# Optimization experiments

Measured on AMD Instinct MI355X. Metric: run time of the kernel, lower is better.

Reference implementation:

```python
import jax, jax.numpy as jnp
import numpy as np

B, T, C = 4, 2048, 1024
E, TOP_K, DFF = 8, 2, 4096


def setup_inputs() -> dict:
    key = jax.random.key(0)
    ks = jax.random.split(key, 8)
    scale = 0.02
    return {
        "x": jax.random.normal(ks[0], (B, T, C), dtype=jnp.float32),
        "noise": jax.random.normal(ks[1], (B, T, E), dtype=jnp.float32),
        "w_gate": jax.random.normal(ks[2], (C, E), dtype=jnp.float32) * scale,
        "b_gate": jnp.zeros((E,), dtype=jnp.float32),
        "w_noise": jax.random.normal(ks[3], (C, E), dtype=jnp.float32) * scale,
        "b_noise": jnp.zeros((E,), dtype=jnp.float32),
        "w1": jax.random.normal(ks[4], (E, C, DFF), dtype=jnp.float32) * scale,
        "b1": jnp.zeros((E, DFF), dtype=jnp.float32),
        "w2": jax.random.normal(ks[5], (E, DFF, C), dtype=jnp.float32) * scale,
        "b2": jnp.zeros((E, C), dtype=jnp.float32),
    }


def reference(x, noise, w_gate, b_gate, w_noise, b_noise, w1, b1, w2, b2):
    # Noisy top-k router
    clean_logits = jnp.einsum("btc,ce->bte", x, w_gate) + b_gate
    noise_logits = jnp.einsum("btc,ce->bte", x, w_noise) + b_noise
    logits = clean_logits + noise * jax.nn.softplus(noise_logits)  # (B,T,E)
    top_v, top_i = jax.lax.top_k(logits, TOP_K)  # (B,T,K)
    # softmax over sparse (-inf elsewhere) logits == softmax over top-k values
    # scattered back to expert slots
    w_topk = jax.nn.softmax(top_v, axis=-1)  # (B,T,K)
    weights = jnp.einsum("btk,btke->bte", w_topk, jax.nn.one_hot(top_i, E, dtype=x.dtype))

    # Dense-equivalent dispatch/combine: weights are exactly 0 for
    # non-selected experts, so weighted dense compute matches the
    # gather/scatter combine in the original module.
    out = jnp.zeros_like(x)
    n_experts = w1.shape[0]
    for e in range(n_experts):
        h = jax.nn.relu(jnp.einsum("btc,cf->btf", x, w1[e]) + b1[e])
        y = jnp.einsum("btf,fc->btc", h, w2[e]) + b2[e]
        out = out + weights[..., e:e + 1] * y
    return out
```

## Files before the change

### kernel.cpp

```cpp
#include <hip/hip_runtime.h>
#include <hip/hip_bf16.h>
#include <cmath>

#define DEVFN __device__ __forceinline__

typedef __attribute__((ext_vector_type(8))) short short8;
typedef __attribute__((ext_vector_type(4))) float f32x4;

constexpr int C_DIM   = 1024;
constexpr int E_NUM   = 8;
constexpr int DFF_DIM = 4096;
constexpr int NTOK    = 8192;
constexpr int PAD     = 256;
constexpr int MAXROWS = NTOK * 2 + E_NUM * PAD;

DEVFN unsigned short f2bf(float f) {
    __hip_bfloat16 h = __float2bfloat16(f);
    return __builtin_bit_cast(unsigned short, h);
}
DEVFN float bf2f(unsigned short u) {
    return __bfloat162float(__builtin_bit_cast(__hip_bfloat16, u));
}
DEVFN void gload_lds16(const void* g, void* lds) {
    __builtin_amdgcn_global_load_lds(
        (const __attribute__((address_space(1))) unsigned int*)g,
        (__attribute__((address_space(3))) unsigned int*)lds, 16, 0, 0);
}


__global__ void init_kernel(int* meta, int* rowtok,
                            const float* __restrict__ wg, const float* __restrict__ wn,
                            float* __restrict__ wT) {
    int gid = blockIdx.x * 256 + threadIdx.x;
    if (gid < 64) meta[gid] = 0;
    if (gid < MAXROWS) rowtok[gid] = 0;
    if (gid < 16 * C_DIM) {
        int o = gid >> 10, c = gid & 1023;
        wT[gid] = (o < 8) ? wg[c * 8 + o] : wn[c * 8 + (o - 8)];
    }
}

__global__ __launch_bounds__(256) void router_kernel(
    const float* __restrict__ x, const float* __restrict__ noise,
    const float* __restrict__ wT, const float* __restrict__ bg,
    const float* __restrict__ bn, int* meta, int2* tok_e, float2* tok_w) {
    extern __shared__ float swT[];
    int tid = threadIdx.x;
#pragma unroll
    for (int j = 0; j < 16; j++) {
        int idx = (j * 256 + tid) * 4;
        *(float4*)&swT[idx] = *(const float4*)&wT[idx];
    }
    __syncthreads();

    int tt = tid >> 3, sub = tid & 7;
    int tok = blockIdx.x * 32 + tt;
    const float* xr = x + (size_t)tok * C_DIM;

    double acc[16];
#pragma unroll
    for (int o = 0; o < 16; o++) acc[o] = 0.0;

#pragma unroll 4
    for (int i = 0; i < 32; i++) {
        int c = i * 32 + sub * 4;
        float4 xv = *(const float4*)(xr + c);
#pragma unroll
        for (int o = 0; o < 16; o++) {
            float4 wv = *(const float4*)(&swT[o * C_DIM + c]);
            acc[o] += (double)xv.x * (double)wv.x;
            acc[o] += (double)xv.y * (double)wv.y;
            acc[o] += (double)xv.z * (double)wv.z;
            acc[o] += (double)xv.w * (double)wv.w;
        }
    }
#pragma unroll
    for (int s = 1; s <= 4; s <<= 1) {
#pragma unroll
        for (int o = 0; o < 16; o++) acc[o] += __shfl_xor(acc[o], s, 64);
    }
    if (sub == 0) {
        double logit[8];
#pragma unroll
        for (int e = 0; e < 8; e++) {
            double cl = acc[e] + (double)bg[e];
            double nl = acc[8 + e] + (double)bn[e];
            double sp = (nl > 30.0) ? nl : log1p(exp(nl));
            logit[e] = cl + (double)noise[(size_t)tok * 8 + e] * sp;
        }
        int i1 = -1, i2 = -1;
        double v1 = -1e300, v2 = -1e300;
#pragma unroll
        for (int e = 0; e < 8; e++) {
            double v = logit[e];
            if (v > v1) { v2 = v1; i2 = i1; v1 = v; i1 = e; }
            else if (v > v2) { v2 = v; i2 = e; }
        }
        double d = exp(v2 - v1);
        tok_e[tok] = make_int2(i1, i2);
        tok_w[tok] = make_float2((float)(1.0 / (1.0 + d)), (float)(d / (1.0 + d)));
        atomicAdd(&meta[i1], 1);
        atomicAdd(&meta[i2], 1);
    }
}

__global__ void offsets_kernel(int* meta) {
    if (threadIdx.x == 0 && blockIdx.x == 0) {
        int off = 0;
        for (int e = 0; e < 8; e++) {
            meta[16 + e] = off;
            off += (meta[e] + PAD - 1) / PAD * PAD;
            meta[8 + e] = 0;
        }
        meta[24] = off;
    }
}

__global__ void assign_kernel(int* meta, const int2* tok_e,
                              int2* tok_pos, int* rowtok) {
    int t = blockIdx.x * 256 + threadIdx.x;
    int lane = threadIdx.x & 63;
    int2 e = tok_e[t];
    int sel[2] = {e.x, e.y};
    int pos[2];
#pragma unroll
    for (int s = 0; s < 2; s++) {
        int p = 0;
#pragma unroll
        for (int ex = 0; ex < 8; ex++) {
            unsigned long long m = __ballot(sel[s] == ex);
            if (m) {
                int leader = __ffsll((unsigned long long)m) - 1;
                int base = 0;
                if (lane == leader) base = atomicAdd(&meta[8 + ex], (int)__popcll(m));
                base = __shfl(base, leader, 64);
                if (sel[s] == ex)
                    p = meta[16 + ex] + base + (int)__popcll(m & ((1ull << lane) - 1ull));
            }
        }
        pos[s] = p;
        rowtok[p] = t;
    }
    tok_pos[t] = make_int2(pos[0], pos[1]);
}

DEVFN void transpose_body(const float* __restrict__ ine, unsigned short* __restrict__ oute,
                          int R, int S, int r0, int s0, float (*tile)[68]) {
    int tid = threadIdx.x;
    int rr = tid >> 2, cs = (tid & 3) * 16;
    const float4* src = (const float4*)(ine + (size_t)(r0 + rr) * S + s0 + cs);
#pragma unroll
    for (int q = 0; q < 4; q++) *(float4*)&tile[rr][cs + q * 4] = src[q];
    __syncthreads();
    int ss = tid >> 2, rs = (tid & 3) * 16;
    ushort4 o[4];
#pragma unroll
    for (int q = 0; q < 4; q++) {
        ushort4 v;
        v.x = f2bf(tile[rs + q * 4 + 0][ss]);
        v.y = f2bf(tile[rs + q * 4 + 1][ss]);
        v.z = f2bf(tile[rs + q * 4 + 2][ss]);
        v.w = f2bf(tile[rs + q * 4 + 3][ss]);
        o[q] = v;
    }
    ushort4* dst = (ushort4*)(oute + (size_t)(s0 + ss) * R + r0 + rs);
#pragma unroll
    for (int q = 0; q < 4; q++) dst[q] = o[q];
}

constexpr int NB_T1 = (DFF_DIM / 64) * (C_DIM / 64) * E_NUM;
constexpr int NB_T2 = (C_DIM / 64) * (DFF_DIM / 64) * E_NUM;
__global__ __launch_bounds__(256) void prep_kernel(
    const float* __restrict__ w1, unsigned short* __restrict__ w1b,
    const float* __restrict__ w2, unsigned short* __restrict__ w2b,
    const float* __restrict__ x, const int* __restrict__ rowtok,
    unsigned short* __restrict__ Xg) {
    __shared__ float tile[64][68];
    int b = blockIdx.x;
    if (b < NB_T1) {
        int bx = b & 63, by = (b >> 6) & 15, bz = b >> 10;
        transpose_body(w1 + (size_t)bz * C_DIM * DFF_DIM,
                       w1b + (size_t)bz * C_DIM * DFF_DIM,
                       C_DIM, DFF_DIM, by * 64, bx * 64, tile);
        return;
    }
    b -= NB_T1;
    if (b < NB_T2) {
        int bx = b & 15, by = (b >> 4) & 63, bz = b >> 10;
        transpose_body(w2 + (size_t)bz * C_DIM * DFF_DIM,
                       w2b + (size_t)bz * C_DIM * DFF_DIM,
                       DFF_DIM, C_DIM, by * 64, bx * 64, tile);
        return;
    }
    b -= NB_T2;
    int tok = rowtok[b];
    const float4* src = (const float4*)(x + (size_t)tok * C_DIM);
    ushort4* dst = (ushort4*)(Xg + (size_t)b * C_DIM);
    int i = threadIdx.x;
    float4 v = src[i];
    ushort4 o;
    o.x = f2bf(v.x); o.y = f2bf(v.y); o.z = f2bf(v.z); o.w = f2bf(v.w);
    dst[i] = o;
}

template <int KDIM, int KLEN, int NDIM, int MODE>
__global__ __launch_bounds__(512, 2) void gemm8_kernel(
    const unsigned short* __restrict__ A, const unsigned short* __restrict__ Bt,
    const float* __restrict__ bias, unsigned short* __restrict__ OutH,
    unsigned short* __restrict__ OutC0, unsigned short* __restrict__ OutC1,
    const int* __restrict__ meta) {
    extern __shared__ char ldsraw[];

    int nwg = gridDim.x;
    int orig = blockIdx.x;
    int q = nwg >> 3, r8 = nwg & 7;
    int xcd = orig & 7, idx = orig >> 3;
    int wgid = (xcd < r8 ? xcd * (q + 1) : r8 * (q + 1) + (xcd - r8) * q) + idx;
    constexpr int NCT = NDIM / 256;
    int rowBase = (wgid / NCT) * 256;
    int colBase = (wgid % NCT) * 256;
    if (rowBase >= meta[24]) return;
    int e = 0;
#pragma unroll
    for (int i = 1; i < 8; i++)
        if (rowBase >= meta[16 + i]) e = i;
    int koff = blockIdx.z * KLEN;

    int tid = threadIdx.x;
    int wv = tid >> 6, lane = tid & 63;
    int wr = wv >> 2, wcol = wv & 3;

    const unsigned short* Ab = A + (size_t)rowBase * KDIM + koff;
    const unsigned short* Bb = Bt + (size_t)e * NDIM * KDIM + (size_t)colBase * KDIM + koff;

    int rA = tid >> 3;
    int sSl = ((tid & 7) ^ (rA & 7)) * 8;
    const unsigned short* pA0 = Ab + (size_t)rA * KDIM + sSl;
    const unsigned short* pB0 = Bb + (size_t)rA * KDIM + sSl;

#define STAGEALL(tt) { \
        char* base_ = ldsraw + (((tt) & 1) << 16); \
        size_t kadd_ = (size_t)(tt) * 64; \
        _Pragma("unroll") for (int h_ = 0; h_ < 2; h_++) { \
            char* dA_ = base_ + h_ * 16384 + wv * 1024; \
            const unsigned short* sA_ = pA0 + (size_t)h_ * (128 * KDIM) + kadd_; \
            gload_lds16(sA_, dA_); \
            gload_lds16(sA_ + (size_t)64 * KDIM, dA_ + 8192); \
            char* dB_ = base_ + 32768 + h_ * 16384 + wv * 1024; \
            const unsigned short* sB_ = pB0 + (size_t)h_ * (128 * KDIM) + kadd_; \
            gload_lds16(sB_, dB_); \
            gload_lds16(sB_ + (size_t)64 * KDIM, dB_ + 8192); \
        } }

    int physk0 = (lane >> 4) ^ (lane & 7);
    int kdel = ((physk0 ^ 4) - physk0) * 16;
    const char* aB0k0 = ldsraw + wr * 16384 + (lane & 15) * 128 + physk0 * 16;
    const char* aB0k1 = aB0k0 + kdel;
    const char* bB0k0 = ldsraw + 32768 + (wcol >> 1) * 16384 +
                        ((wcol & 1) * 64 + (lane & 15)) * 128 + physk0 * 16;
    const char* bB0k1 = bB0k0 + kdel;

    short8 afA[4][2], afB[4][2], bfA[2][2], bfB[2][2];
    f32x4 acc[8][4];
#pragma unroll
    for (int m = 0; m < 8; m++)
#pragma unroll
        for (int n = 0; n < 4; n++) acc[m][n] = f32x4{0.f, 0.f, 0.f, 0.f};

#define LDA(DST, K0, K1, MOFF) \
    _Pragma("unroll") for (int mm = 0; mm < 4; mm++) { \
        DST[mm][0] = *(const short8*)((K0) + ((MOFF) + mm) * 2048); \
        DST[mm][1] = *(const short8*)((K1) + ((MOFF) + mm) * 2048); }
#define LDB(DST, K0, K1, NOFF) \
    _Pragma("unroll") for (int nn = 0; nn < 2; nn++) { \
        DST[nn][0] = *(const short8*)((K0) + ((NOFF) + nn) * 2048); \
        DST[nn][1] = *(const short8*)((K1) + ((NOFF) + nn) * 2048); }
#define QUAD(AF, BF, MB, NB) \
    __builtin_amdgcn_s_setprio(1); \
    _Pragma("unroll") for (int kk = 0; kk < 2; kk++) \
    _Pragma("unroll") for (int mm = 0; mm < 4; mm++) \
    _Pragma("unroll") for (int nn = 0; nn < 2; nn++) \
        acc[(MB) + mm][(NB) + nn] = __builtin_amdgcn_mfma_f32_16x16x32_bf16( \
            AF[mm][kk], BF[nn][kk], acc[(MB) + mm][(NB) + nn], 0, 0, 0); \
    __builtin_amdgcn_s_setprio(0);
#define SB() __builtin_amdgcn_sched_barrier(0)

    constexpr int T = KLEN / 64;

    STAGEALL(0)
    SB(); asm volatile("s_waitcnt vmcnt(0)" ::: "memory"); SB();
    __builtin_amdgcn_s_barrier(); SB();

#pragma unroll 1
    for (int t = 0; t < T; ++t) {
        if (t + 1 < T) STAGEALL(t + 1)
        const char* ak0 = aB0k0 + ((t & 1) << 16);
        const char* ak1 = aB0k1 + ((t & 1) << 16);
        const char* bk0 = bB0k0 + ((t & 1) << 16);
        const char* bk1 = bB0k1 + ((t & 1) << 16);
        LDA(afA, ak0, ak1, 0)
        LDB(bfA, bk0, bk1, 0)
        LDB(bfB, bk0, bk1, 2)
        QUAD(afA, bfA, 0, 0)
        LDA(afB, ak0, ak1, 4)
        QUAD(afA, bfB, 0, 2)
        QUAD(afB, bfA, 4, 0)
        QUAD(afB, bfB, 4, 2)
        SB();
        asm volatile("s_waitcnt vmcnt(0)" ::: "memory");
        SB();
        __builtin_amdgcn_s_barrier();
        SB();
    }
#undef STAGEALL
#undef LDA
#undef LDB
#undef QUAD

    float bv[4];
    bool addBias = (MODE == 1) || (blockIdx.z == 0);
#pragma unroll
    for (int n = 0; n < 4; n++)
        bv[n] = addBias ? bias[(size_t)e * NDIM + colBase + wcol * 64 + n * 16 + (lane & 15)]
                        : 0.f;
    unsigned short* OutP = (MODE == 1) ? OutH : (blockIdx.z == 0 ? OutC0 : OutC1);

    unsigned short* lds16 = (unsigned short*)ldsraw;
#pragma unroll
    for (int m = 0; m < 8; m++) {
#pragma unroll
        for (int n = 0; n < 4; n++) {
#pragma unroll
            for (int j = 0; j < 4; j++) {
                float v = acc[m][n][j] + bv[n];
                if (MODE == 1) v = fmaxf(v, 0.f);
                int rr = wr * 128 + m * 16 + (lane >> 4) * 4 + j;
                int cc = wcol * 64 + n * 16 + (lane & 15);
                lds16[rr * 256 + (cc ^ ((rr & 7) << 4))] = f2bf(v);
            }
        }
    }
    __syncthreads();
    {
        int row = tid >> 1, half = tid & 1;
        int xr = (row & 7) << 4;
#pragma unroll
        for (int i = 0; i < 16; i++) {
            int cs = half * 128 + i * 8;
            short8 val = *(const short8*)(lds16 + row * 256 + (cs ^ xr));
            *(short8*)(OutP + (size_t)(rowBase + row) * NDIM + colBase + cs) = val;
        }
    }
}

__global__ void combine_kernel(const unsigned short* __restrict__ c0,
                               const unsigned short* __restrict__ c1,
                               const int2* __restrict__ tok_pos, const float2* __restrict__ tok_w,
                               float* __restrict__ out) {
    int t = blockIdx.x;
    int2 p = tok_pos[t];
    float2 w = tok_w[t];
    int i = threadIdx.x;
    ushort4 a0 = ((const ushort4*)(c0 + (size_t)p.x * C_DIM))[i];
    ushort4 a1 = ((const ushort4*)(c1 + (size_t)p.x * C_DIM))[i];
    ushort4 b0 = ((const ushort4*)(c0 + (size_t)p.y * C_DIM))[i];
    ushort4 b1 = ((const ushort4*)(c1 + (size_t)p.y * C_DIM))[i];
    float4 r;
    r.x = w.x * (bf2f(a0.x) + bf2f(a1.x)) + w.y * (bf2f(b0.x) + bf2f(b1.x));
    r.y = w.x * (bf2f(a0.y) + bf2f(a1.y)) + w.y * (bf2f(b0.y) + bf2f(b1.y));
    r.z = w.x * (bf2f(a0.z) + bf2f(a1.z)) + w.y * (bf2f(b0.z) + bf2f(b1.z));
    r.w = w.x * (bf2f(a0.w) + bf2f(a1.w)) + w.y * (bf2f(b0.w) + bf2f(b1.w));
    ((float4*)(out + (size_t)t * C_DIM))[i] = r;
}

extern "C" void kernel_launch(void* const* d_in, const int* in_sizes, int n_in,
                              void* d_out, int out_size, void* d_ws, size_t ws_size,
                              hipStream_t stream) {
    (void)in_sizes; (void)n_in; (void)out_size; (void)ws_size;
    const float* x       = (const float*)d_in[0];
    const float* noise   = (const float*)d_in[1];
    const float* w_gate  = (const float*)d_in[2];
    const float* b_gate  = (const float*)d_in[3];
    const float* w_noise = (const float*)d_in[4];
    const float* b_noise = (const float*)d_in[5];
    const float* w1      = (const float*)d_in[6];
    const float* b1      = (const float*)d_in[7];
    const float* w2      = (const float*)d_in[8];
    const float* b2      = (const float*)d_in[9];
    float* out = (float*)d_out;

    char* w = (char*)d_ws;
    size_t off = 0;
    int* meta = (int*)(w + off); off += 256;
    float* wT = (float*)(w + off); off += 16 * C_DIM * 4;
    int2* tok_e = (int2*)(w + off); off += (size_t)NTOK * 8;
    float2* tok_w = (float2*)(w + off); off += (size_t)NTOK * 8;
    int2* tok_pos = (int2*)(w + off); off += (size_t)NTOK * 8;
    int* rowtok = (int*)(w + off); off += (size_t)MAXROWS * 4;
    unsigned short* H = (unsigned short*)(w + off); off += (size_t)MAXROWS * DFF_DIM * 2;
    unsigned short* w2b = (unsigned short*)(w + off); off += (size_t)E_NUM * C_DIM * DFF_DIM * 2;
    unsigned short* c0 = (unsigned short*)(w + off); off += (size_t)MAXROWS * C_DIM * 2;
    unsigned short* Xg = (unsigned short*)(w + off); off += (size_t)MAXROWS * C_DIM * 2;
    unsigned short* w1b = (unsigned short*)(w + off); off += (size_t)E_NUM * DFF_DIM * C_DIM * 2;
    unsigned short* c1 = Xg;

    init_kernel<<<(MAXROWS + 255) / 256, 256, 0, stream>>>(meta, rowtok, w_gate, w_noise, wT);

    hipFuncSetAttribute((const void*)router_kernel,
                        hipFuncAttributeMaxDynamicSharedMemorySize, 65536);
    router_kernel<<<NTOK / 32, 256, 65536, stream>>>(x, noise, wT, b_gate, b_noise,
                                                     meta, tok_e, tok_w);
    offsets_kernel<<<1, 64, 0, stream>>>(meta);
    assign_kernel<<<NTOK / 256, 256, 0, stream>>>(meta, tok_e, tok_pos, rowtok);
    prep_kernel<<<NB_T1 + NB_T2 + MAXROWS, 256, 0, stream>>>(w1, w1b, w2, w2b, x, rowtok, Xg);

    hipFuncSetAttribute((const void*)gemm8_kernel<C_DIM, C_DIM, DFF_DIM, 1>,
                        hipFuncAttributeMaxDynamicSharedMemorySize, 131072);
    gemm8_kernel<C_DIM, C_DIM, DFF_DIM, 1>
        <<<dim3((MAXROWS / 256) * (DFF_DIM / 256), 1, 1), 512, 131072, stream>>>(
            Xg, w1b, b1, H, nullptr, nullptr, meta);

    hipFuncSetAttribute((const void*)gemm8_kernel<DFF_DIM, DFF_DIM / 2, C_DIM, 2>,
                        hipFuncAttributeMaxDynamicSharedMemorySize, 131072);
    gemm8_kernel<DFF_DIM, DFF_DIM / 2, C_DIM, 2>
        <<<dim3((MAXROWS / 256) * (C_DIM / 256), 1, 2), 512, 131072, stream>>>(
            H, w2b, b2, nullptr, c0, c1, meta);

    combine_kernel<<<NTOK, 256, 0, stream>>>(c0, c1, tok_pos, tok_w, out);
}
```

Baseline: 633.8 us.

## Use 4-wave 256x256 GEMM tiles with 128x128 per wave and 4-way split-K

Cuts the expert GEMM workgroup from 8 waves to 4, so each wave computes a 128x128 output sub-tile with an 8x8 grid of MFMA accumulators, raising fragment reuse per LDS read. Staging loops are rewritten for 256 threads, and the second GEMM's split-K goes from 2 to 4 slices, with two more partial buffers and a combine kernel that sums four partials. This trades occupancy and latency hiding (256 accumulator registers per lane, one workgroup per CU) for fewer LDS reads per MFMA and more parallelism in the second GEMM, at the cost of extra partial-sum traffic.

```diff
diff --git a/kernel.cpp b/kernel.cpp
--- a/kernel.cpp
+++ b/kernel.cpp
@@ -204,10 +204,11 @@
 }
 
 template <int KDIM, int KLEN, int NDIM, int MODE>
-__global__ __launch_bounds__(512, 2) void gemm8_kernel(
+__global__ __launch_bounds__(256, 1) void gemm8_kernel(
     const unsigned short* __restrict__ A, const unsigned short* __restrict__ Bt,
     const float* __restrict__ bias, unsigned short* __restrict__ OutH,
     unsigned short* __restrict__ OutC0, unsigned short* __restrict__ OutC1,
+    unsigned short* __restrict__ OutC2, unsigned short* __restrict__ OutC3,
     const int* __restrict__ meta) {
     extern __shared__ char ldsraw[];
 
@@ -228,7 +229,7 @@
 
     int tid = threadIdx.x;
     int wv = tid >> 6, lane = tid & 63;
-    int wr = wv >> 2, wcol = wv & 3;
+    int wr = wv >> 1, wc = wv & 1;
 
     const unsigned short* Ab = A + (size_t)rowBase * KDIM + koff;
     const unsigned short* Bb = Bt + (size_t)e * NDIM * KDIM + (size_t)colBase * KDIM + koff;
@@ -241,48 +242,25 @@
 #define STAGEALL(tt) { \
         char* base_ = ldsraw + (((tt) & 1) << 16); \
         size_t kadd_ = (size_t)(tt) * 64; \
-        _Pragma("unroll") for (int h_ = 0; h_ < 2; h_++) { \
-            char* dA_ = base_ + h_ * 16384 + wv * 1024; \
-            const unsigned short* sA_ = pA0 + (size_t)h_ * (128 * KDIM) + kadd_; \
-            gload_lds16(sA_, dA_); \
-            gload_lds16(sA_ + (size_t)64 * KDIM, dA_ + 8192); \
-            char* dB_ = base_ + 32768 + h_ * 16384 + wv * 1024; \
-            const unsigned short* sB_ = pB0 + (size_t)h_ * (128 * KDIM) + kadd_; \
-            gload_lds16(sB_, dB_); \
-            gload_lds16(sB_ + (size_t)64 * KDIM, dB_ + 8192); \
+        _Pragma("unroll") for (int j_ = 0; j_ < 8; j_++) { \
+            gload_lds16(pA0 + (size_t)j_ * 32 * KDIM + kadd_, \
+                        base_ + j_ * 4096 + wv * 1024); \
+            gload_lds16(pB0 + (size_t)j_ * 32 * KDIM + kadd_, \
+                        base_ + 32768 + j_ * 4096 + wv * 1024); \
         } }
 
     int physk0 = (lane >> 4) ^ (lane & 7);
     int kdel = ((physk0 ^ 4) - physk0) * 16;
     const char* aB0k0 = ldsraw + wr * 16384 + (lane & 15) * 128 + physk0 * 16;
-    const char* aB0k1 = aB0k0 + kdel;
-    const char* bB0k0 = ldsraw + 32768 + (wcol >> 1) * 16384 +
-                        ((wcol & 1) * 64 + (lane & 15)) * 128 + physk0 * 16;
-    const char* bB0k1 = bB0k0 + kdel;
-
-    short8 afA[4][2], afB[4][2], bfA[2][2], bfB[2][2];
-    f32x4 acc[8][4];
+    const char* bB0k0 = ldsraw + 32768 + wc * 16384 + (lane & 15) * 128 + physk0 * 16;
+
+    short8 af[8], bf[8];
+    f32x4 acc[8][8];
 #pragma unroll
     for (int m = 0; m < 8; m++)
 #pragma unroll
-        for (int n = 0; n < 4; n++) acc[m][n] = f32x4{0.f, 0.f, 0.f, 0.f};
-
-#define LDA(DST, K0, K1, MOFF) \
-    _Pragma("unroll") for (int mm = 0; mm < 4; mm++) { \
-        DST[mm][0] = *(const short8*)((K0) + ((MOFF) + mm) * 2048); \
-        DST[mm][1] = *(const short8*)((K1) + ((MOFF) + mm) * 2048); }
-#define LDB(DST, K0, K1, NOFF) \
-    _Pragma("unroll") for (int nn = 0; nn < 2; nn++) { \
-        DST[nn][0] = *(const short8*)((K0) + ((NOFF) + nn) * 2048); \
-        DST[nn][1] = *(const short8*)((K1) + ((NOFF) + nn) * 2048); }
-#define QUAD(AF, BF, MB, NB) \
-    __builtin_amdgcn_s_setprio(1); \
-    _Pragma("unroll") for (int kk = 0; kk < 2; kk++) \
-    _Pragma("unroll") for (int mm = 0; mm < 4; mm++) \
-    _Pragma("unroll") for (int nn = 0; nn < 2; nn++) \
-        acc[(MB) + mm][(NB) + nn] = __builtin_amdgcn_mfma_f32_16x16x32_bf16( \
-            AF[mm][kk], BF[nn][kk], acc[(MB) + mm][(NB) + nn], 0, 0, 0); \
-    __builtin_amdgcn_s_setprio(0);
+        for (int n = 0; n < 8; n++) acc[m][n] = f32x4{0.f, 0.f, 0.f, 0.f};
+
 #define SB() __builtin_amdgcn_sched_barrier(0)
 
     constexpr int T = KLEN / 64;
@@ -294,18 +272,25 @@
 #pragma unroll 1
     for (int t = 0; t < T; ++t) {
         if (t + 1 < T) STAGEALL(t + 1)
-        const char* ak0 = aB0k0 + ((t & 1) << 16);
-        const char* ak1 = aB0k1 + ((t & 1) << 16);
-        const char* bk0 = bB0k0 + ((t & 1) << 16);
-        const char* bk1 = bB0k1 + ((t & 1) << 16);
-        LDA(afA, ak0, ak1, 0)
-        LDB(bfA, bk0, bk1, 0)
-        LDB(bfB, bk0, bk1, 2)
-        QUAD(afA, bfA, 0, 0)
-        LDA(afB, ak0, ak1, 4)
-        QUAD(afA, bfB, 0, 2)
-        QUAD(afB, bfA, 4, 0)
-        QUAD(afB, bfB, 4, 2)
+        const char* ab = aB0k0 + ((t & 1) << 16);
+        const char* bb = bB0k0 + ((t & 1) << 16);
+#pragma unroll
+        for (int kk = 0; kk < 2; kk++) {
+            const char* ak = ab + kk * kdel;
+            const char* bk = bb + kk * kdel;
+#pragma unroll
+            for (int m = 0; m < 8; m++) af[m] = *(const short8*)(ak + m * 2048);
+#pragma unroll
+            for (int n = 0; n < 8; n++) bf[n] = *(const short8*)(bk + n * 2048);
+            __builtin_amdgcn_s_setprio(1);
+#pragma unroll
+            for (int m = 0; m < 8; m++)
+#pragma unroll
+                for (int n = 0; n < 8; n++)
+                    acc[m][n] = __builtin_amdgcn_mfma_f32_16x16x32_bf16(
+                        af[m], bf[n], acc[m][n], 0, 0, 0);
+            __builtin_amdgcn_s_setprio(0);
+        }
         SB();
         asm volatile("s_waitcnt vmcnt(0)" ::: "memory");
         SB();
@@ -313,40 +298,39 @@
         SB();
     }
 #undef STAGEALL
-#undef LDA
-#undef LDB
-#undef QUAD
-
-    float bv[4];
+
+    float bv[8];
     bool addBias = (MODE == 1) || (blockIdx.z == 0);
 #pragma unroll
-    for (int n = 0; n < 4; n++)
-        bv[n] = addBias ? bias[(size_t)e * NDIM + colBase + wcol * 64 + n * 16 + (lane & 15)]
+    for (int n = 0; n < 8; n++)
+        bv[n] = addBias ? bias[(size_t)e * NDIM + colBase + wc * 128 + n * 16 + (lane & 15)]
                         : 0.f;
-    unsigned short* OutP = (MODE == 1) ? OutH : (blockIdx.z == 0 ? OutC0 : OutC1);
+    unsigned short* OutP = (MODE == 1) ? OutH
+                         : (blockIdx.z == 0 ? OutC0 : blockIdx.z == 1 ? OutC1
+                         : blockIdx.z == 2 ? OutC2 : OutC3);
 
     unsigned short* lds16 = (unsigned short*)ldsraw;
 #pragma unroll
     for (int m = 0; m < 8; m++) {
 #pragma unroll
-        for (int n = 0; n < 4; n++) {
+        for (int n = 0; n < 8; n++) {
 #pragma unroll
             for (int j = 0; j < 4; j++) {
                 float v = acc[m][n][j] + bv[n];
                 if (MODE == 1) v = fmaxf(v, 0.f);
                 int rr = wr * 128 + m * 16 + (lane >> 4) * 4 + j;
-                int cc = wcol * 64 + n * 16 + (lane & 15);
+                int cc = wc * 128 + n * 16 + (lane & 15);
                 lds16[rr * 256 + (cc ^ ((rr & 7) << 4))] = f2bf(v);
             }
         }
     }
     __syncthreads();
     {
-        int row = tid >> 1, half = tid & 1;
+        int row = tid;
         int xr = (row & 7) << 4;
 #pragma unroll
-        for (int i = 0; i < 16; i++) {
-            int cs = half * 128 + i * 8;
+        for (int i = 0; i < 32; i++) {
+            int cs = i * 8;
             short8 val = *(const short8*)(lds16 + row * 256 + (cs ^ xr));
             *(short8*)(OutP + (size_t)(rowBase + row) * NDIM + colBase + cs) = val;
         }
@@ -355,21 +339,32 @@
 
 __global__ void combine_kernel(const unsigned short* __restrict__ c0,
                                const unsigned short* __restrict__ c1,
+                               const unsigned short* __restrict__ c2,
+                               const unsigned short* __restrict__ c3,
                                const int2* __restrict__ tok_pos, const float2* __restrict__ tok_w,
                                float* __restrict__ out) {
     int t = blockIdx.x;
     int2 p = tok_pos[t];
     float2 w = tok_w[t];
     int i = threadIdx.x;
-    ushort4 a0 = ((const ushort4*)(c0 + (size_t)p.x * C_DIM))[i];
-    ushort4 a1 = ((const ushort4*)(c1 + (size_t)p.x * C_DIM))[i];
-    ushort4 b0 = ((const ushort4*)(c0 + (size_t)p.y * C_DIM))[i];
-    ushort4 b1 = ((const ushort4*)(c1 + (size_t)p.y * C_DIM))[i];
+    size_t o0 = (size_t)p.x * C_DIM, o1 = (size_t)p.y * C_DIM;
+    ushort4 a0 = ((const ushort4*)(c0 + o0))[i];
+    ushort4 a1 = ((const ushort4*)(c1 + o0))[i];
+    ushort4 a2 = ((const ushort4*)(c2 + o0))[i];
+    ushort4 a3 = ((const ushort4*)(c3 + o0))[i];
+    ushort4 b0 = ((const ushort4*)(c0 + o1))[i];
+    ushort4 b1 = ((const ushort4*)(c1 + o1))[i];
+    ushort4 b2 = ((const ushort4*)(c2 + o1))[i];
+    ushort4 b3 = ((const ushort4*)(c3 + o1))[i];
     float4 r;
-    r.x = w.x * (bf2f(a0.x) + bf2f(a1.x)) + w.y * (bf2f(b0.x) + bf2f(b1.x));
-    r.y = w.x * (bf2f(a0.y) + bf2f(a1.y)) + w.y * (bf2f(b0.y) + bf2f(b1.y));
-    r.z = w.x * (bf2f(a0.z) + bf2f(a1.z)) + w.y * (bf2f(b0.z) + bf2f(b1.z));
-    r.w = w.x * (bf2f(a0.w) + bf2f(a1.w)) + w.y * (bf2f(b0.w) + bf2f(b1.w));
+    r.x = w.x * (bf2f(a0.x) + bf2f(a1.x) + bf2f(a2.x) + bf2f(a3.x))
+        + w.y * (bf2f(b0.x) + bf2f(b1.x) + bf2f(b2.x) + bf2f(b3.x));
+    r.y = w.x * (bf2f(a0.y) + bf2f(a1.y) + bf2f(a2.y) + bf2f(a3.y))
+        + w.y * (bf2f(b0.y) + bf2f(b1.y) + bf2f(b2.y) + bf2f(b3.y));
+    r.z = w.x * (bf2f(a0.z) + bf2f(a1.z) + bf2f(a2.z) + bf2f(a3.z))
+        + w.y * (bf2f(b0.z) + bf2f(b1.z) + bf2f(b2.z) + bf2f(b3.z));
+    r.w = w.x * (bf2f(a0.w) + bf2f(a1.w) + bf2f(a2.w) + bf2f(a3.w))
+        + w.y * (bf2f(b0.w) + bf2f(b1.w) + bf2f(b2.w) + bf2f(b3.w));
     ((float4*)(out + (size_t)t * C_DIM))[i] = r;
 }
 
@@ -402,7 +397,9 @@
     unsigned short* c0 = (unsigned short*)(w + off); off += (size_t)MAXROWS * C_DIM * 2;
     unsigned short* Xg = (unsigned short*)(w + off); off += (size_t)MAXROWS * C_DIM * 2;
     unsigned short* w1b = (unsigned short*)(w + off); off += (size_t)E_NUM * DFF_DIM * C_DIM * 2;
+    unsigned short* c3 = (unsigned short*)(w + off); off += (size_t)MAXROWS * C_DIM * 2;
     unsigned short* c1 = Xg;
+    unsigned short* c2 = w1b;
 
     init_kernel<<<(MAXROWS + 255) / 256, 256, 0, stream>>>(meta, rowtok, w_gate, w_noise, wT);
 
@@ -417,14 +414,14 @@
     hipFuncSetAttribute((const void*)gemm8_kernel<C_DIM, C_DIM, DFF_DIM, 1>,
                         hipFuncAttributeMaxDynamicSharedMemorySize, 131072);
     gemm8_kernel<C_DIM, C_DIM, DFF_DIM, 1>
-        <<<dim3((MAXROWS / 256) * (DFF_DIM / 256), 1, 1), 512, 131072, stream>>>(
-            Xg, w1b, b1, H, nullptr, nullptr, meta);
-
-    hipFuncSetAttribute((const void*)gemm8_kernel<DFF_DIM, DFF_DIM / 2, C_DIM, 2>,
+        <<<dim3((MAXROWS / 256) * (DFF_DIM / 256), 1, 1), 256, 131072, stream>>>(
+            Xg, w1b, b1, H, nullptr, nullptr, nullptr, nullptr, meta);
+
+    hipFuncSetAttribute((const void*)gemm8_kernel<DFF_DIM, DFF_DIM / 4, C_DIM, 2>,
                         hipFuncAttributeMaxDynamicSharedMemorySize, 131072);
-    gemm8_kernel<DFF_DIM, DFF_DIM / 2, C_DIM, 2>
-        <<<dim3((MAXROWS / 256) * (C_DIM / 256), 1, 2), 512, 131072, stream>>>(
-            H, w2b, b2, nullptr, c0, c1, meta);
-
-    combine_kernel<<<NTOK, 256, 0, stream>>>(c0, c1, tok_pos, tok_w, out);
-}
+    gemm8_kernel<DFF_DIM, DFF_DIM / 4, C_DIM, 2>
+        <<<dim3((MAXROWS / 256) * (C_DIM / 256), 1, 4), 256, 131072, stream>>>(
+            H, w2b, b2, nullptr, c0, c1, c2, c3, meta);
+
+    combine_kernel<<<NTOK, 256, 0, stream>>>(c0, c1, c2, c3, tok_pos, tok_w, out);
+}
```

Result: slower. 877.4 us (+38.4%).

## Gather token rows inside first GEMM via rowtok instead of pre-gathered Xg

Applied to the files above, without the earlier changes.

The prep kernel now converts x to bf16 once per token instead of materialising a padded, gathered Xg buffer of MAXROWS rows. The first expert GEMM looks up row indices from rowtok and loads A rows indirectly, which removes one gather-write pass over memory. The transpose store is also widened to two 16-byte vector stores. The trade-off is indirect, less contiguous A loads in the GEMM, padded rows reading whatever token rowtok holds for them, and a separate c1 buffer.

```diff
diff --git a/kernel.cpp b/kernel.cpp
--- a/kernel.cpp
+++ b/kernel.cpp
@@ -153,19 +153,14 @@
     for (int q = 0; q < 4; q++) *(float4*)&tile[rr][cs + q * 4] = src[q];
     __syncthreads();
     int ss = tid >> 2, rs = (tid & 3) * 16;
-    ushort4 o[4];
-#pragma unroll
-    for (int q = 0; q < 4; q++) {
-        ushort4 v;
-        v.x = f2bf(tile[rs + q * 4 + 0][ss]);
-        v.y = f2bf(tile[rs + q * 4 + 1][ss]);
-        v.z = f2bf(tile[rs + q * 4 + 2][ss]);
-        v.w = f2bf(tile[rs + q * 4 + 3][ss]);
-        o[q] = v;
-    }
-    ushort4* dst = (ushort4*)(oute + (size_t)(s0 + ss) * R + r0 + rs);
-#pragma unroll
-    for (int q = 0; q < 4; q++) dst[q] = o[q];
+    short8 v0, v1;
+#pragma unroll
+    for (int q = 0; q < 8; q++) v0[q] = (short)f2bf(tile[rs + q][ss]);
+#pragma unroll
+    for (int q = 0; q < 8; q++) v1[q] = (short)f2bf(tile[rs + 8 + q][ss]);
+    unsigned short* dst = oute + (size_t)(s0 + ss) * R + r0 + rs;
+    *(short8*)dst = v0;
+    *(short8*)(dst + 8) = v1;
 }
 
 constexpr int NB_T1 = (DFF_DIM / 64) * (C_DIM / 64) * E_NUM;
@@ -173,8 +168,7 @@
 __global__ __launch_bounds__(256) void prep_kernel(
     const float* __restrict__ w1, unsigned short* __restrict__ w1b,
     const float* __restrict__ w2, unsigned short* __restrict__ w2b,
-    const float* __restrict__ x, const int* __restrict__ rowtok,
-    unsigned short* __restrict__ Xg) {
+    const float* __restrict__ x, unsigned short* __restrict__ xb) {
     __shared__ float tile[64][68];
     int b = blockIdx.x;
     if (b < NB_T1) {
@@ -193,9 +187,8 @@
         return;
     }
     b -= NB_T2;
-    int tok = rowtok[b];
-    const float4* src = (const float4*)(x + (size_t)tok * C_DIM);
-    ushort4* dst = (ushort4*)(Xg + (size_t)b * C_DIM);
+    const float4* src = (const float4*)(x + (size_t)b * C_DIM);
+    ushort4* dst = (ushort4*)(xb + (size_t)b * C_DIM);
     int i = threadIdx.x;
     float4 v = src[i];
     ushort4 o;
@@ -203,12 +196,12 @@
     dst[i] = o;
 }
 
-template <int KDIM, int KLEN, int NDIM, int MODE>
+template <int KDIM, int KLEN, int NDIM, int MODE, bool INDIR>
 __global__ __launch_bounds__(512, 2) void gemm8_kernel(
     const unsigned short* __restrict__ A, const unsigned short* __restrict__ Bt,
     const float* __restrict__ bias, unsigned short* __restrict__ OutH,
     unsigned short* __restrict__ OutC0, unsigned short* __restrict__ OutC1,
-    const int* __restrict__ meta) {
+    const int* __restrict__ meta, const int* __restrict__ rowtok) {
     extern __shared__ char ldsraw[];
 
     int nwg = gridDim.x;
@@ -230,26 +223,31 @@
     int wv = tid >> 6, lane = tid & 63;
     int wr = wv >> 2, wcol = wv & 3;
 
-    const unsigned short* Ab = A + (size_t)rowBase * KDIM + koff;
     const unsigned short* Bb = Bt + (size_t)e * NDIM * KDIM + (size_t)colBase * KDIM + koff;
 
     int rA = tid >> 3;
     int sSl = ((tid & 7) ^ (rA & 7)) * 8;
-    const unsigned short* pA0 = Ab + (size_t)rA * KDIM + sSl;
+    const unsigned short* pA[4];
+    if constexpr (INDIR) {
+#pragma unroll
+        for (int j = 0; j < 4; j++) {
+            int tok = rowtok[rowBase + rA + j * 64];
+            pA[j] = A + (size_t)tok * KDIM + sSl + koff;
+        }
+    } else {
+        const unsigned short* pA0 = A + (size_t)(rowBase + rA) * KDIM + sSl + koff;
+#pragma unroll
+        for (int j = 0; j < 4; j++) pA[j] = pA0 + (size_t)j * 64 * KDIM;
+    }
     const unsigned short* pB0 = Bb + (size_t)rA * KDIM + sSl;
 
 #define STAGEALL(tt) { \
         char* base_ = ldsraw + (((tt) & 1) << 16); \
         size_t kadd_ = (size_t)(tt) * 64; \
-        _Pragma("unroll") for (int h_ = 0; h_ < 2; h_++) { \
-            char* dA_ = base_ + h_ * 16384 + wv * 1024; \
-            const unsigned short* sA_ = pA0 + (size_t)h_ * (128 * KDIM) + kadd_; \
-            gload_lds16(sA_, dA_); \
-            gload_lds16(sA_ + (size_t)64 * KDIM, dA_ + 8192); \
-            char* dB_ = base_ + 32768 + h_ * 16384 + wv * 1024; \
-            const unsigned short* sB_ = pB0 + (size_t)h_ * (128 * KDIM) + kadd_; \
-            gload_lds16(sB_, dB_); \
-            gload_lds16(sB_ + (size_t)64 * KDIM, dB_ + 8192); \
+        _Pragma("unroll") for (int j_ = 0; j_ < 4; j_++) { \
+            gload_lds16(pA[j_] + kadd_, base_ + j_ * 8192 + wv * 1024); \
+            gload_lds16(pB0 + (size_t)j_ * 64 * KDIM + kadd_, \
+                        base_ + 32768 + j_ * 8192 + wv * 1024); \
         } }
 
     int physk0 = (lane >> 4) ^ (lane & 7);
@@ -400,9 +398,9 @@
     unsigned short* H = (unsigned short*)(w + off); off += (size_t)MAXROWS * DFF_DIM * 2;
     unsigned short* w2b = (unsigned short*)(w + off); off += (size_t)E_NUM * C_DIM * DFF_DIM * 2;
     unsigned short* c0 = (unsigned short*)(w + off); off += (size_t)MAXROWS * C_DIM * 2;
-    unsigned short* Xg = (unsigned short*)(w + off); off += (size_t)MAXROWS * C_DIM * 2;
+    unsigned short* c1 = (unsigned short*)(w + off); off += (size_t)MAXROWS * C_DIM * 2;
+    unsigned short* xb = (unsigned short*)(w + off); off += (size_t)NTOK * C_DIM * 2;
     unsigned short* w1b = (unsigned short*)(w + off); off += (size_t)E_NUM * DFF_DIM * C_DIM * 2;
-    unsigned short* c1 = Xg;
 
     init_kernel<<<(MAXROWS + 255) / 256, 256, 0, stream>>>(meta, rowtok, w_gate, w_noise, wT);
 
@@ -412,19 +410,19 @@
                                                      meta, tok_e, tok_w);
     offsets_kernel<<<1, 64, 0, stream>>>(meta);
     assign_kernel<<<NTOK / 256, 256, 0, stream>>>(meta, tok_e, tok_pos, rowtok);
-    prep_kernel<<<NB_T1 + NB_T2 + MAXROWS, 256, 0, stream>>>(w1, w1b, w2, w2b, x, rowtok, Xg);
-
-    hipFuncSetAttribute((const void*)gemm8_kernel<C_DIM, C_DIM, DFF_DIM, 1>,
+    prep_kernel<<<NB_T1 + NB_T2 + NTOK, 256, 0, stream>>>(w1, w1b, w2, w2b, x, xb);
+
+    hipFuncSetAttribute((const void*)gemm8_kernel<C_DIM, C_DIM, DFF_DIM, 1, true>,
                         hipFuncAttributeMaxDynamicSharedMemorySize, 131072);
-    gemm8_kernel<C_DIM, C_DIM, DFF_DIM, 1>
+    gemm8_kernel<C_DIM, C_DIM, DFF_DIM, 1, true>
         <<<dim3((MAXROWS / 256) * (DFF_DIM / 256), 1, 1), 512, 131072, stream>>>(
-            Xg, w1b, b1, H, nullptr, nullptr, meta);
-
-    hipFuncSetAttribute((const void*)gemm8_kernel<DFF_DIM, DFF_DIM / 2, C_DIM, 2>,
+            xb, w1b, b1, H, nullptr, nullptr, meta, rowtok);
+
+    hipFuncSetAttribute((const void*)gemm8_kernel<DFF_DIM, DFF_DIM / 2, C_DIM, 2, false>,
                         hipFuncAttributeMaxDynamicSharedMemorySize, 131072);
-    gemm8_kernel<DFF_DIM, DFF_DIM / 2, C_DIM, 2>
+    gemm8_kernel<DFF_DIM, DFF_DIM / 2, C_DIM, 2, false>
         <<<dim3((MAXROWS / 256) * (C_DIM / 256), 1, 2), 512, 131072, stream>>>(
-            H, w2b, b2, nullptr, c0, c1, meta);
+            H, w2b, b2, nullptr, c0, c1, meta, nullptr);
 
     combine_kernel<<<NTOK, 256, 0, stream>>>(c0, c1, tok_pos, tok_w, out);
 }
```

Result: no change. 626.3 us (-1.2%).
